# Performance work log

Measured on AMD Instinct MI355X. Metric: run time of the kernel, lower is better.

Reference implementation:

```python
import jax, jax.numpy as jnp
import numpy as np

B, T, X, H, Z, Y, G = 4096, 32, 256, 256, 128, 2, 128


def setup_inputs() -> dict:
    key = jax.random.key(0)
    ks = jax.random.split(key, 16)
    rn = lambda k, s, sc=0.05: jax.random.normal(k, s, dtype=jnp.float32) * sc
    n_days = jnp.concatenate([jnp.array([T], dtype=jnp.int32),
                              jax.random.randint(ks[2], (B - 1,), 1, T + 1).astype(jnp.int32)])
    return {
        "x": rn(ks[0], (B, T, X), 1.0),
        "y_true": jax.nn.softmax(jax.random.normal(ks[1], (B, T, Y), dtype=jnp.float32), axis=-1),
        "n_days": n_days,
        "z0": rn(ks[3], (B, Z), 1.0),
        "eps": rn(ks[4], (T, B, Z), 1.0),
        "W_ih": rn(ks[5], (3 * H, X)), "W_hh": rn(ks[6], (3 * H, H)),
        "b_ih": jnp.zeros((3 * H,), jnp.float32), "b_hh": jnp.zeros((3 * H,), jnp.float32),
        "Wph": rn(ks[7], (Z, X + H + Z)), "bph": jnp.zeros((Z,), jnp.float32),
        "Woh": rn(ks[8], (Z, X + H + Y + Z)), "boh": jnp.zeros((Z,), jnp.float32),
        "Wpm": rn(ks[9], (Z, Z)), "bpm": jnp.zeros((Z,), jnp.float32),
        "Wps": rn(ks[10], (Z, Z)), "bps": jnp.zeros((Z,), jnp.float32),
        "Wqm": rn(ks[11], (Z, Z)), "bqm": jnp.zeros((Z,), jnp.float32),
        "Wqs": rn(ks[12], (Z, Z)), "bqs": jnp.zeros((Z,), jnp.float32),
        "Wg": rn(ks[13], (G, H + Z)), "bg": jnp.zeros((G,), jnp.float32),
        "Wy": rn(ks[14], (Y, G)), "by": jnp.zeros((Y,), jnp.float32),
    }


def _forward(x, y_true, z0, eps, W_ih, W_hh, b_ih, b_hh, Wph, bph, Woh, boh,
             Wpm, bpm, Wps, bps, Wqm, bqm, Wqs, bqs, Wg, bg, Wy, by, n_days):
    xt = jnp.transpose(x, (1, 0, 2))       # [T, B, X]
    yt = jnp.transpose(y_true, (1, 0, 2))  # [T, B, Y]

    # --- GRU over time (torch nn.GRU gate math) ---
    def gru_step(h, xi):
        gi = xi @ W_ih.T + b_ih
        gh = h @ W_hh.T + b_hh
        ir, iz, inn = jnp.split(gi, 3, axis=-1)
        hr, hz, hn = jnp.split(gh, 3, axis=-1)
        r = jax.nn.sigmoid(ir + hr)
        u = jax.nn.sigmoid(iz + hz)
        n = jnp.tanh(inn + r * hn)
        h_new = (1.0 - u) * n + u * h
        return h_new, h_new

    h0 = jnp.zeros((x.shape[0], H), x.dtype)
    _, hs = jax.lax.scan(gru_step, h0, xt)  # [T, B, H]
    # pack/pad semantics: padded timesteps produce zero outputs
    valid = jnp.arange(T)[:, None] < n_days[None, :]  # [T, B]
    hs = jnp.where(valid[:, :, None], hs, 0.0)

    # --- sequential VAE latent scan: z_t depends on z_{t-1} ---
    def vmd_step(z, inputs):
        xi, hi, yi, ei = inputs
        hzp = jnp.tanh(jnp.concatenate([xi, hi, z], -1) @ Wph.T + bph)
        mp = hzp @ Wpm.T + bpm
        sp = jnp.sqrt(jnp.exp(hzp @ Wps.T + bps))
        hzq = jnp.tanh(jnp.concatenate([xi, hi, yi, z], -1) @ Woh.T + boh)
        mq = hzq @ Wqm.T + bqm
        sq = jnp.sqrt(jnp.exp(hzq @ Wqs.T + bqs))
        z_post = mq + sq * ei
        # kl_normal_normal(post || prior)
        kl = jnp.log(sp / sq) + (sq * sq + (mq - mp) ** 2) / (2.0 * sp * sp) - 0.5
        return z_post, (z_post, kl)

    _, (z_posts, kls_e) = jax.lax.scan(vmd_step, z0, (xt, hs, yt, eps))
    kls = jnp.sum(kls_e, axis=-1).T  # [B, T]

    hz = jnp.concatenate([jnp.transpose(hs, (1, 0, 2)),
                          jnp.transpose(z_posts, (1, 0, 2))], -1)  # [B, T, H+Z]
    g = jnp.tanh(hz @ Wg.T + bg)                     # [B, T, G]
    y_pred = jax.nn.softmax(g @ Wy.T + by, axis=-1)  # [B, T, Y]

    idx = n_days - 1
    b = jnp.arange(x.shape[0])
    g_T = g[b, idx]       # [B, G]
    y_T = y_pred[b, idx]  # [B, Y]
    return jnp.concatenate([g_T, y_T, kls], axis=-1)  # [B, G+Y+T]


def reference(x, y_true, n_days, z0, eps, W_ih, W_hh, b_ih, b_hh, Wph, bph,
              Woh, boh, Wpm, bpm, Wps, bps, Wqm, bqm, Wqs, bqs, Wg, bg, Wy, by):
    return _forward(x, y_true, z0, eps, W_ih, W_hh, b_ih, b_hh, Wph, bph, Woh,
                    boh, Wpm, bpm, Wps, bps, Wqm, bqm, Wqs, bqs, Wg, bg, Wy, by,
                    n_days)
```

## Files before the change

### kernel.cpp

```cpp
#include <hip/hip_runtime.h>

typedef unsigned short u16;
typedef short bf16x8 __attribute__((ext_vector_type(8)));
typedef float f32x4 __attribute__((ext_vector_type(4)));

__device__ __forceinline__ float bf2f(u16 v){
  union { unsigned u; float f; } x; x.u = ((unsigned)v) << 16; return x.f;
}
__device__ __forceinline__ u16 f2bf(float f){
  union { float f; unsigned u; } x; x.f = f;
  unsigned u = x.u;
  u += 0x7fffu + ((u >> 16) & 1u);
  return (u16)(u >> 16);
}
__device__ __forceinline__ unsigned pk_bf16(float lo, float hi){
  unsigned r;
  asm("v_cvt_pk_bf16_f32 %0, %1, %2" : "=v"(r) : "v"(lo), "v"(hi));
  return r;
}
__device__ __forceinline__ u16 el4(ushort4 v, int r){ return r==0?v.x:r==1?v.y:r==2?v.z:v.w; }
__device__ __forceinline__ float elf4(float4 v, int r){ return r==0?v.x:r==1?v.y:r==2?v.z:v.w; }
__device__ __forceinline__ float sigm(float x){ return 1.f/(1.f+__expf(-x)); }
__device__ __forceinline__ float tanh_s(float x){ return 1.f - 2.f/(__expf(2.f*x)+1.f); }
__device__ __forceinline__ f32x4 mfma16(bf16x8 a, bf16x8 b, f32x4 c){
  return __builtin_amdgcn_mfma_f32_16x16x32_bf16(a, b, c, 0, 0, 0);
}
__device__ __forceinline__ void gl2lds16(const void* g, void* l){
  __builtin_amdgcn_global_load_lds(
      (const __attribute__((address_space(1))) unsigned int*)g,
      (__attribute__((address_space(3))) unsigned int*)l, 16, 0, 0);
}

__global__ void prep_w(const float* __restrict__ W_ih, const float* __restrict__ W_hh,
                       const float* __restrict__ Wph, const float* __restrict__ Woh,
                       const float* __restrict__ Wpm, const float* __restrict__ Wps,
                       const float* __restrict__ Wqm, const float* __restrict__ Wqs,
                       const float* __restrict__ Wg,  const float* __restrict__ bph,
                       const float* __restrict__ boh,
                       u16* __restrict__ wsb, float* __restrict__ Woy, float* __restrict__ bpq)
{
  int idx = blockIdx.x*256 + threadIdx.x;
  if (idx < 196608){ wsb[idx] = f2bf(W_ih[idx]); return; }
  if (idx < 393216){ wsb[idx] = f2bf(W_hh[idx-196608]); return; }
  if (idx < 524288){ int j = idx-393216; int row = j>>9, col = j&511;
    float v = (row<128) ? Wph[row*640+col] : Woh[(row-128)*642+col];
    wsb[idx] = f2bf(v); return; }
  if (idx < 540672){ int j = idx-524288; int row=j>>7, col=j&127; wsb[idx]=f2bf(Wph[row*640+512+col]); return; }
  if (idx < 557056){ int j = idx-540672; int row=j>>7, col=j&127; wsb[idx]=f2bf(Woh[row*642+514+col]); return; }
  if (idx < 573440){ wsb[idx]=f2bf(Wpm[idx-557056]); return; }
  if (idx < 589824){ wsb[idx]=f2bf(Wps[idx-573440]); return; }
  if (idx < 606208){ wsb[idx]=f2bf(Wqm[idx-589824]); return; }
  if (idx < 622592){ wsb[idx]=f2bf(Wqs[idx-606208]); return; }
  if (idx < 671744){ wsb[idx]=f2bf(Wg[idx-622592]); return; }
  if (idx < 672000){ int j = idx-671744; int row=j>>1; Woy[j] = Woh[row*642+512+(j&1)]; return; }
  if (idx < 672256){ int j = idx-672000; bpq[j] = (j<128) ? bph[j] : boh[j-128]; return; }
}

__global__ void prep_b(const float* __restrict__ b_ih, const float* __restrict__ b_hh,
                       float* __restrict__ bsum)
{
  int j = threadIdx.x;
  if (j < 768) bsum[j] = b_ih[j] + (j < 512 ? b_hh[j] : 0.f);
}

__global__ void prep_x(const float* __restrict__ x, u16* __restrict__ xbf){
  int i = blockIdx.x*256 + threadIdx.x;
  if (i >= 4194304) return;
  const float4* src = (const float4*)(x + (size_t)i*8);
  float4 a = src[0], b = src[1];
  uint4 o;
  o.x = pk_bf16(a.x, a.y);
  o.y = pk_bf16(a.z, a.w);
  o.z = pk_bf16(b.x, b.y);
  o.w = pk_bf16(b.z, b.w);
  ((uint4*)xbf)[i] = o;
}

__global__ void sort_days(const int* __restrict__ n_days, int* __restrict__ perm,
                          int* __restrict__ nd_s, int* __restrict__ cnt)
{
  __shared__ int hist[34];
  __shared__ int base[34];
  __shared__ int cursor[34];
  int tid = threadIdx.x;
  if (tid < 34) hist[tid] = 0;
  __syncthreads();
  for (int i = tid; i < 4096; i += 1024) atomicAdd(&hist[n_days[i]], 1);
  __syncthreads();
  if (tid == 0){
    int acc = 0;
    for (int v = 32; v >= 1; --v){ base[v] = acc; acc += hist[v]; }
    base[0] = acc;
  }
  __syncthreads();
  if (tid < 33) cursor[tid] = base[tid];
  if (tid < 32) cnt[tid] = base[tid];
  __syncthreads();
  for (int i = tid; i < 4096; i += 1024){
    int v = n_days[i];
    int pos = atomicAdd(&cursor[v], 1);
    perm[pos] = i;
    nd_s[pos] = v;
  }
}

__global__ __launch_bounds__(512, 4) void gemm_gi(
  const u16* __restrict__ A, const u16* __restrict__ W,
  const float* __restrict__ bias, const int* __restrict__ perm,
  const int* __restrict__ cnt, u16* __restrict__ C)
{
  const int t  = blockIdx.x >> 5;
  const int rt = blockIdx.x & 31;
  if (rt*128 >= cnt[t]) return;
  const int n0 = blockIdx.y*256;
  const int tid = threadIdx.x;
  const int w = tid>>6, lane = tid&63, c = lane&15, g = lane>>4;
  const int wm = w>>2, wn = w&3;
  __shared__ __align__(16) char smem[49152];
  u16* abuf = (u16*)smem;
  u16* wbuf = (u16*)(smem + 16384);
  u16* clds = (u16*)smem;

  size_t asrc[2];
  #pragma unroll
  for (int i=0;i<2;++i){
    int p = (w*2+i)*64 + lane;
    int k8 = p>>7, row = p&127;
    asrc[i] = ((size_t)perm[rt*128 + row]*32 + t)*256 + k8*8;
  }
  size_t wsrc[4];
  #pragma unroll
  for (int i=0;i<4;++i){
    int p = (w*4+i)*64 + lane;
    int k8 = p>>8, row = p&255;
    wsrc[i] = (size_t)(n0+row)*256 + k8*8;
  }
  f32x4 acc[4][4];
  #pragma unroll
  for (int i=0;i<4;++i)
    #pragma unroll
    for (int j=0;j<4;++j) acc[i][j] = (f32x4){0.f,0.f,0.f,0.f};
  for (int kc=0; kc<4; ++kc){
    __syncthreads();
    #pragma unroll
    for (int i=0;i<2;++i) gl2lds16(A + asrc[i] + kc*64, &abuf[(w*2+i)*512]);
    #pragma unroll
    for (int i=0;i<4;++i) gl2lds16(W + wsrc[i] + kc*64, &wbuf[(w*4+i)*512]);
    __syncthreads();
    #pragma unroll
    for (int ks=0;ks<2;++ks){
      int k8 = ks*4 + g;
      bf16x8 a[4];
      #pragma unroll
      for (int mt=0;mt<4;++mt) a[mt] = *(const bf16x8*)&abuf[(k8*128 + wm*64 + mt*16 + c)*8];
      #pragma unroll
      for (int nt=0;nt<4;++nt){
        bf16x8 b = *(const bf16x8*)&wbuf[(k8*256 + wn*64 + nt*16 + c)*8];
        #pragma unroll
        for (int mt=0;mt<4;++mt)
          acc[mt][nt] = mfma16(a[mt], b, acc[mt][nt]);
      }
    }
  }
  __syncthreads();
  const size_t crow = (size_t)t*4096 + rt*128;
  #pragma unroll
  for (int nh=0; nh<2; ++nh){
    if ((wn>>1) == nh){
      #pragma unroll
      for (int nt=0;nt<4;++nt){
        int n = n0 + wn*64 + nt*16 + c;
        float bn = bias[n];
        int lc = (wn&1)*64 + nt*16 + c;
        #pragma unroll
        for (int mt=0;mt<4;++mt){
          int lr = wm*64 + mt*16 + g*4;
          #pragma unroll
          for (int r=0;r<4;++r)
            clds[(lr+r)*136 + lc] = f2bf(acc[mt][nt][r] + bn);
        }
      }
    }
    __syncthreads();
    #pragma unroll
    for (int p=0;p<4;++p){
      int idx = p*512 + tid;
      int row = idx>>4, ch = idx&15;
      *(uint4*)(C + (crow+row)*768 + n0 + nh*128 + ch*8)
        = *(const uint4*)&clds[row*136 + ch*8];
    }
    __syncthreads();
  }
}

__global__ __launch_bounds__(512, 4) void gemm_hpq(
  const u16* __restrict__ A1, const u16* __restrict__ A2,
  const u16* __restrict__ W, const float* __restrict__ bias,
  const float* __restrict__ yt, const float* __restrict__ Woy,
  u16* __restrict__ C)
{
  const int m0 = blockIdx.x*128;
  const int tid = threadIdx.x;
  const int w = tid>>6, lane = tid&63, c = lane&15, g = lane>>4;
  const int wm = w>>2, wn = w&3;
  __shared__ __align__(16) char smem[49152];
  u16* abuf = (u16*)smem;
  u16* wbuf = (u16*)(smem + 16384);
  u16* clds = (u16*)smem;

  size_t asrc[2];
  #pragma unroll
  for (int i=0;i<2;++i){
    int p = (w*2+i)*64 + lane;
    int k8 = p>>7, row = p&127;
    asrc[i] = (size_t)(m0+row)*256 + k8*8;
  }
  size_t wsrc[4];
  #pragma unroll
  for (int i=0;i<4;++i){
    int p = (w*4+i)*64 + lane;
    int k8 = p>>8, row = p&255;
    wsrc[i] = (size_t)row*512 + k8*8;
  }
  f32x4 acc[4][4];
  #pragma unroll
  for (int i=0;i<4;++i)
    #pragma unroll
    for (int j=0;j<4;++j) acc[i][j] = (f32x4){0.f,0.f,0.f,0.f};
  for (int kc=0; kc<8; ++kc){
    __syncthreads();
    const u16* Ab = (kc < 4) ? A1 : A2;
    int ko = (kc & 3)*64;
    #pragma unroll
    for (int i=0;i<2;++i) gl2lds16(Ab + asrc[i] + ko, &abuf[(w*2+i)*512]);
    #pragma unroll
    for (int i=0;i<4;++i) gl2lds16(W + wsrc[i] + kc*64, &wbuf[(w*4+i)*512]);
    __syncthreads();
    #pragma unroll
    for (int ks=0;ks<2;++ks){
      int k8 = ks*4 + g;
      bf16x8 a[4];
      #pragma unroll
      for (int mt=0;mt<4;++mt) a[mt] = *(const bf16x8*)&abuf[(k8*128 + wm*64 + mt*16 + c)*8];
      #pragma unroll
      for (int nt=0;nt<4;++nt){
        bf16x8 b = *(const bf16x8*)&wbuf[(k8*256 + wn*64 + nt*16 + c)*8];
        #pragma unroll
        for (int mt=0;mt<4;++mt)
          acc[mt][nt] = mfma16(a[mt], b, acc[mt][nt]);
      }
    }
  }
  __syncthreads();
  #pragma unroll
  for (int nh=0; nh<2; ++nh){
    if ((wn>>1) == nh){
      #pragma unroll
      for (int nt=0;nt<4;++nt){
        int n = wn*64 + nt*16 + c;
        float bn = bias[n];
        float wy0 = 0.f, wy1 = 0.f;
        bool yfl = (n >= 128);
        if (yfl){ wy0 = Woy[(n-128)*2]; wy1 = Woy[(n-128)*2+1]; }
        int lc = (wn&1)*64 + nt*16 + c;
        #pragma unroll
        for (int mt=0;mt<4;++mt){
          int lr = wm*64 + mt*16 + g*4;
          #pragma unroll
          for (int r=0;r<4;++r){
            size_t m = (size_t)m0 + lr + r;
            float v = acc[mt][nt][r] + bn;
            if (yfl) v += yt[2*m]*wy0 + yt[2*m+1]*wy1;
            clds[(lr+r)*136 + lc] = f2bf(v);
          }
        }
      }
    }
    __syncthreads();
    #pragma unroll
    for (int p=0;p<4;++p){
      int idx = p*512 + tid;
      int row = idx>>4, ch = idx&15;
      *(uint4*)(C + (size_t)(m0+row)*256 + nh*128 + ch*8)
        = *(const uint4*)&clds[row*136 + ch*8];
    }
    __syncthreads();
  }
}

__global__ __launch_bounds__(1024) void gru_seq(
  const u16* __restrict__ GI, const u16* __restrict__ Whh,
  const float* __restrict__ bhh, const int* __restrict__ perm,
  const int* __restrict__ nd_s, u16* __restrict__ hs)
{
  const int b0 = blockIdx.x*16;
  const int tid = threadIdx.x;
  const int w = tid>>6, lane = tid&63, c = lane&15, g = lane>>4;
  const int j0 = w*16 + g*4;
  __shared__ __align__(16) u16 hbuf[2][4096];

  bf16x8 wa[3][8];
  #pragma unroll
  for (int gate=0; gate<3; ++gate)
    #pragma unroll
    for (int ks=0; ks<8; ++ks)
      wa[gate][ks] = *(const bf16x8*)&Whh[(size_t)(gate*256 + w*16 + c)*256 + ks*32 + g*8];

  const float4 bhn4 = *(const float4*)(bhh + 512 + j0);
  const int ndc   = nd_s[b0 + c];
  const int bound = nd_s[b0];
  const int ob    = perm[b0 + c];

  const int hroff = (g*16 + c)*16;
  const int hwoff = ((w*2 + (g>>1))*16 + c)*16 + (g&1)*8;
  u16* hsp = hs + (size_t)ob*8192 + j0;
  const size_t PL = 3145728;
  const u16* gib = GI + (size_t)(b0+c)*768 + j0;

  float hprev[4] = {0.f,0.f,0.f,0.f};
  if (tid < 512) ((uint4*)hbuf[0])[tid] = make_uint4(0,0,0,0);

  ushort4 gA[3], gB[3];
  gA[0] = *(const ushort4*)(gib);
  gA[1] = *(const ushort4*)(gib + 256);
  gA[2] = *(const ushort4*)(gib + 512);
  {
    const u16* g1 = gib + ((bound > 1) ? PL : 0);
    gB[0] = *(const ushort4*)(g1);
    gB[1] = *(const ushort4*)(g1 + 256);
    gB[2] = *(const ushort4*)(g1 + 512);
  }
  __syncthreads();

  const u16* hr = hbuf[0];
  u16*       hw = hbuf[1];

  auto step = [&](ushort4 (&gs)[3], int t){
    f32x4 aR = (f32x4){0.f,0.f,0.f,0.f};
    f32x4 aU = (f32x4){0.f,0.f,0.f,0.f};
    f32x4 aN = (f32x4){bhn4.x, bhn4.y, bhn4.z, bhn4.w};
    __builtin_amdgcn_s_setprio(1);
    #pragma unroll
    for (int ks=0; ks<8; ++ks){
      bf16x8 hf = *(const bf16x8*)((const char*)hr + hroff + ks*1024);
      aR = mfma16(wa[0][ks], hf, aR);
      aU = mfma16(wa[1][ks], hf, aU);
      aN = mfma16(wa[2][ks], hf, aN);
    }
    __builtin_amdgcn_s_setprio(0);
    float h4[4];
    #pragma unroll
    for (int r=0; r<4; ++r){
      float rr = sigm(bf2f(el4(gs[0],r)) + aR[r]);
      float uu = sigm(bf2f(el4(gs[1],r)) + aU[r]);
      float nn = tanh_s(bf2f(el4(gs[2],r)) + rr*aN[r]);
      float h = nn + uu*(hprev[r]-nn);
      hprev[r] = h;
      h4[r] = h;
    }
    uint2 hpk;
    hpk.x = pk_bf16(h4[0], h4[1]);
    hpk.y = pk_bf16(h4[2], h4[3]);
    *(uint2*)((char*)hw + hwoff) = hpk;
    *(uint2*)(hsp + t*256) = (t < ndc) ? hpk : make_uint2(0u,0u);
    {
      int pf = (t+2 < bound) ? t+2 : bound-1;
      const u16* gp = gib + (size_t)pf*PL;
      gs[0] = *(const ushort4*)(gp);
      gs[1] = *(const ushort4*)(gp + 256);
      gs[2] = *(const ushort4*)(gp + 512);
    }
    asm volatile("s_waitcnt lgkmcnt(0)" ::: "memory");
    __builtin_amdgcn_sched_barrier(0);
    __builtin_amdgcn_s_barrier();
    __builtin_amdgcn_sched_barrier(0);
    const u16* tmp = hr; hr = hw; hw = (u16*)tmp;
  };

  int t = 0;
  for (;;){
    step(gA, t);
    if (++t >= bound) break;
    step(gB, t);
    if (++t >= bound) break;
  }
  for (int t2 = bound; t2 < 32; ++t2)
    *(uint2*)(hsp + t2*256) = make_uint2(0u,0u);
}

__global__ __launch_bounds__(512) void vae_seq(
  const u16* __restrict__ HPQ, const float* __restrict__ z0,
  const float* __restrict__ eps, const int* __restrict__ n_days,
  const u16* __restrict__ Wm,
  const float* __restrict__ bpm, const float* __restrict__ bps,
  const float* __restrict__ bqm, const float* __restrict__ bqs,
  u16* __restrict__ zidx, float* __restrict__ out)
{
  const int b0 = blockIdx.x*16;
  const int tid = threadIdx.x, w = tid>>6, lane = tid&63, c = lane&15, g = lane>>4;
  const int j0 = w*16 + g*4;
  __shared__ __align__(16) u16 zbuf[16*16*8];
  __shared__ __align__(16) u16 hzpb[16*16*8];
  __shared__ __align__(16) u16 hzqb[16*16*8];
  __shared__ float klb[32][16][8];

  bf16x8 wf[6][4];
  #pragma unroll
  for (int mat=0;mat<6;++mat)
    #pragma unroll
    for (int ks=0;ks<4;++ks)
      wf[mat][ks] = *(const bf16x8*)&Wm[mat*16384 + (w*16+c)*128 + ks*32 + g*8];

  const float4 bpm4 = *(const float4*)(bpm + j0);
  const float4 bps4 = *(const float4*)(bps + j0);
  const float4 bqm4 = *(const float4*)(bqm + j0);
  const float4 bqs4 = *(const float4*)(bqs + j0);
  const int ndc = n_days[b0 + c];

  const int hroff = (g*16 + c)*16;
  const int hwoff = ((w*2 + (g>>1))*16 + c)*16 + (g&1)*8;
  const u16*  hbp = HPQ + ((size_t)(b0+c)*32)*256 + j0;
  const float* ebp = eps + (size_t)(b0+c)*128 + j0;

  if (tid < 256){
    int k8 = tid>>4, row = tid&15;
    const float* zp = z0 + (size_t)(b0+row)*128 + k8*8;
    uint4 o;
    o.x = pk_bf16(zp[0], zp[1]);
    o.y = pk_bf16(zp[2], zp[3]);
    o.z = pk_bf16(zp[4], zp[5]);
    o.w = pk_bf16(zp[6], zp[7]);
    ((uint4*)zbuf)[tid] = o;
  }
  __syncthreads();

  ushort4 pA = *(const ushort4*)(hbp);
  ushort4 qA = *(const ushort4*)(hbp + 128);
  float4  eA = *(const float4*)(ebp);
  ushort4 pB = *(const ushort4*)(hbp + 256);
  ushort4 qB = *(const ushort4*)(hbp + 384);
  float4  eB = *(const float4*)(ebp + 524288);

  uint2 zsel = make_uint2(0u,0u);

  auto step = [&](ushort4& hp4, ushort4& hq4, float4& e4, int t){
    f32x4 accP = (f32x4){0,0,0,0}, accQ = (f32x4){0,0,0,0};
    #pragma unroll
    for (int ks=0;ks<4;++ks){
      bf16x8 zf = *(const bf16x8*)((const char*)zbuf + hroff + ks*1024);
      accP = mfma16(wf[0][ks], zf, accP);
      accQ = mfma16(wf[1][ks], zf, accQ);
    }
    float p4[4], q4[4];
    #pragma unroll
    for (int r=0;r<4;++r){
      p4[r] = tanh_s(bf2f(el4(hp4,r)) + accP[r]);
      q4[r] = tanh_s(bf2f(el4(hq4,r)) + accQ[r]);
    }
    uint2 ppk, qpk;
    ppk.x = pk_bf16(p4[0], p4[1]);  ppk.y = pk_bf16(p4[2], p4[3]);
    qpk.x = pk_bf16(q4[0], q4[1]);  qpk.y = pk_bf16(q4[2], q4[3]);
    *(uint2*)((char*)hzpb + hwoff) = ppk;
    *(uint2*)((char*)hzqb + hwoff) = qpk;
    asm volatile("s_waitcnt lgkmcnt(0)" ::: "memory");
    __builtin_amdgcn_sched_barrier(0);
    __builtin_amdgcn_s_barrier();
    __builtin_amdgcn_sched_barrier(0);
    f32x4 aMP=(f32x4){0,0,0,0}, aAP=(f32x4){0,0,0,0};
    f32x4 aMQ=(f32x4){0,0,0,0}, aAQ=(f32x4){0,0,0,0};
    #pragma unroll
    for (int ks=0;ks<4;++ks){
      bf16x8 pf = *(const bf16x8*)((const char*)hzpb + hroff + ks*1024);
      bf16x8 qf = *(const bf16x8*)((const char*)hzqb + hroff + ks*1024);
      aMP = mfma16(wf[2][ks], pf, aMP);
      aAP = mfma16(wf[3][ks], pf, aAP);
      aMQ = mfma16(wf[4][ks], qf, aMQ);
      aAQ = mfma16(wf[5][ks], qf, aAQ);
    }
    float kls = 0.f;
    float z4[4];
    #pragma unroll
    for (int r=0;r<4;++r){
      float mp = aMP[r]+elf4(bpm4,r);
      float ap = aAP[r]+elf4(bps4,r);
      float mq = aMQ[r]+elf4(bqm4,r);
      float aq = aAQ[r]+elf4(bqs4,r);
      float ev = elf4(e4,r);
      float z = mq + __expf(0.5f*aq)*ev;
      float d = mq - mp;
      kls += 0.5f*(ap-aq) + 0.5f*(__expf(aq)+d*d)*__expf(-ap) - 0.5f;
      z4[r] = z;
    }
    uint2 zpk;
    zpk.x = pk_bf16(z4[0], z4[1]);
    zpk.y = pk_bf16(z4[2], z4[3]);
    *(uint2*)((char*)zbuf + hwoff) = zpk;
    if (t == ndc-1) zsel = zpk;
    kls += __shfl_xor(kls, 16);
    kls += __shfl_xor(kls, 32);
    if (lane < 16) klb[t][c][w] = kls;
    if (t < 30){
      hp4 = *(const ushort4*)(hbp + (t+2)*256);
      hq4 = *(const ushort4*)(hbp + (t+2)*256 + 128);
      e4  = *(const float4*)(ebp + (size_t)(t+2)*524288);
    }
    asm volatile("s_waitcnt lgkmcnt(0)" ::: "memory");
    __builtin_amdgcn_sched_barrier(0);
    __builtin_amdgcn_s_barrier();
    __builtin_amdgcn_sched_barrier(0);
  };

  #pragma unroll 1
  for (int t=0; t<32; t+=2){
    step(pA, qA, eA, t);
    step(pB, qB, eB, t+1);
  }

  *(uint2*)(zidx + (size_t)(b0+c)*128 + j0) = zsel;
  {
    int t2 = tid>>4, c2 = tid&15;
    float s = 0.f;
    #pragma unroll
    for (int ww=0;ww<8;++ww) s += klb[t2][c2][ww];
    out[(size_t)(b0+c2)*162 + 130 + t2] = s;
  }
}

__global__ __launch_bounds__(128) void head_k(
  const u16* __restrict__ hs, const u16* __restrict__ zidx,
  const int* __restrict__ n_days, const u16* __restrict__ Wgb,
  const float* __restrict__ bg, const float* __restrict__ Wy,
  const float* __restrict__ by, float* __restrict__ out)
{
  const int b = blockIdx.x;
  const int tid = threadIdx.x;
  const int lane = tid & 63, wv = tid >> 6;
  __shared__ float hz[384];
  __shared__ float red[2][2];
  const int idx = n_days[b]-1;
  const u16* hrow = hs + ((size_t)b*32 + idx)*256;
  for (int k=tid; k<256; k+=128) hz[k] = bf2f(hrow[k]);
  hz[256+tid] = bf2f(zidx[(size_t)b*128 + tid]);
  __syncthreads();
  const u16* wrow = Wgb + (size_t)tid*384;
  float s = 0.f;
  #pragma unroll 4
  for (int k8=0;k8<48;++k8){
    bf16x8 wvv = *(const bf16x8*)&wrow[k8*8];
    #pragma unroll
    for (int e=0;e<8;++e) s += bf2f((u16)wvv[e]) * hz[k8*8+e];
  }
  float gv = tanh_s(s + bg[tid]);
  out[(size_t)b*162 + tid] = gv;
  float a0 = gv*Wy[tid], a1 = gv*Wy[128+tid];
  #pragma unroll
  for (int off=1; off<64; off<<=1){
    a0 += __shfl_xor(a0, off);
    a1 += __shfl_xor(a1, off);
  }
  if (lane == 0){ red[0][wv] = a0; red[1][wv] = a1; }
  __syncthreads();
  if (tid == 0){
    float l0 = by[0] + red[0][0] + red[0][1];
    float l1 = by[1] + red[1][0] + red[1][1];
    float mx = fmaxf(l0,l1);
    float e0 = __expf(l0-mx), e1 = __expf(l1-mx);
    float si = e0+e1;
    out[(size_t)b*162 + 128] = e0/si;
    out[(size_t)b*162 + 129] = e1/si;
  }
}

extern "C" void kernel_launch(void* const* d_in, const int* in_sizes, int n_in,
                              void* d_out, int out_size, void* d_ws, size_t ws_size,
                              hipStream_t stream)
{
  const float* x      = (const float*)d_in[0];
  const float* y_true = (const float*)d_in[1];
  const int*   n_days = (const int*)d_in[2];
  const float* z0     = (const float*)d_in[3];
  const float* eps    = (const float*)d_in[4];
  const float* W_ih   = (const float*)d_in[5];
  const float* W_hh   = (const float*)d_in[6];
  const float* b_ih   = (const float*)d_in[7];
  const float* b_hh   = (const float*)d_in[8];
  const float* Wph    = (const float*)d_in[9];
  const float* bph    = (const float*)d_in[10];
  const float* Woh    = (const float*)d_in[11];
  const float* boh    = (const float*)d_in[12];
  const float* Wpm    = (const float*)d_in[13];
  const float* bpm    = (const float*)d_in[14];
  const float* Wps    = (const float*)d_in[15];
  const float* bps    = (const float*)d_in[16];
  const float* Wqm    = (const float*)d_in[17];
  const float* bqm    = (const float*)d_in[18];
  const float* Wqs    = (const float*)d_in[19];
  const float* bqs    = (const float*)d_in[20];
  const float* Wg     = (const float*)d_in[21];
  const float* bg     = (const float*)d_in[22];
  const float* Wy     = (const float*)d_in[23];
  const float* by     = (const float*)d_in[24];
  (void)in_sizes; (void)n_in; (void)out_size; (void)ws_size;

  u16*   wsb = (u16*)d_ws;
  float* wsf = (float*)d_ws;
  int*   wsi = (int*)d_ws;
  u16* Wih_b = wsb + 0;
  u16* Whh_b = wsb + 196608;
  u16* Wc_b  = wsb + 393216;
  u16* Wz_b  = wsb + 524288;
  u16* Wg_b  = wsb + 622592;
  float* Woy  = wsf + 335872;
  float* bpq  = wsf + 336128;
  float* bsum = wsf + 336384;
  int* perm   = wsi + 337152;
  int* nd_s   = wsi + 341248;
  int* cnt    = wsi + 345344;
  u16* xbf   = wsb + 690752;
  u16* GI    = wsb + 34245184;
  u16* hsB   = wsb + 134908480;
  u16* HPQ   = wsb + 168462912;
  u16* zidx  = wsb + 202017344;

  hipLaunchKernelGGL(prep_w, dim3(2626), dim3(256), 0, stream,
                     W_ih, W_hh, Wph, Woh, Wpm, Wps, Wqm, Wqs, Wg, bph, boh,
                     wsb, Woy, bpq);
  hipLaunchKernelGGL(prep_b, dim3(1), dim3(768), 0, stream, b_ih, b_hh, bsum);
  hipLaunchKernelGGL(prep_x, dim3(16384), dim3(256), 0, stream, x, xbf);
  hipLaunchKernelGGL(sort_days, dim3(1), dim3(1024), 0, stream,
                     n_days, perm, nd_s, cnt);
  hipLaunchKernelGGL(gemm_gi, dim3(1024,3), dim3(512), 0, stream,
                     xbf, Wih_b, bsum, perm, cnt, GI);
  hipLaunchKernelGGL(gru_seq, dim3(256), dim3(1024), 0, stream,
                     GI, Whh_b, b_hh, perm, nd_s, hsB);
  hipLaunchKernelGGL(gemm_hpq, dim3(1024), dim3(512), 0, stream,
                     xbf, hsB, Wc_b, bpq, y_true, Woy, HPQ);
  hipLaunchKernelGGL(vae_seq, dim3(256), dim3(512), 0, stream,
                     HPQ, z0, eps, n_days, Wz_b, bpm, bps, bqm, bqs, zidx, (float*)d_out);
  hipLaunchKernelGGL(head_k, dim3(4096), dim3(128), 0, stream,
                     hsB, zidx, n_days, Wg_b, bg, Wy, by, (float*)d_out);
}
```

Baseline: 537.3 us.

## Coalesce GRU hidden-state stores via LDS readback and XOR-swizzle hbuf

The GRU kernel no longer writes each thread's scattered 4-element fragment of h to global memory. At the start of the next step each wave reads back one full batch row from the shared h buffer and writes it contiguously, so the stores are coalesced. The final step is flushed after the loop. The shared h buffer layout is XOR-swizzled on both the read and write sides to reduce LDS bank conflicts. This adds an extra LDS read per step and makes the indexing more complex. The vae_seq changes only rename variables and leave the behaviour the same.

```diff
diff --git a/kernel.cpp b/kernel.cpp
--- a/kernel.cpp
+++ b/kernel.cpp
@@ -307,13 +307,20 @@
       wa[gate][ks] = *(const bf16x8*)&Whh[(size_t)(gate*256 + w*16 + c)*256 + ks*32 + g*8];
 
   const float4 bhn4 = *(const float4*)(bhh + 512 + j0);
-  const int ndc   = nd_s[b0 + c];
   const int bound = nd_s[b0];
-  const int ob    = perm[b0 + c];
-
-  const int hroff = (g*16 + c)*16;
-  const int hwoff = ((w*2 + (g>>1))*16 + c)*16 + (g&1)*8;
-  u16* hsp = hs + (size_t)ob*8192 + j0;
+  const int ob_w  = perm[b0 + w];
+  const int ndc_w = nd_s[b0 + w];
+
+  const int hroffE = g*256 + ((c*16) ^ (g<<4));
+  const int hroffO = g*256 + ((c*16) ^ ((4+g)<<4));
+  {
+  }
+  const int hwk8  = w*2 + (g>>1);
+  const int hwoff = (hwk8*256 + c*16 + (g&1)*8) ^ ((hwk8&7)<<4);
+  const int rsk8  = lane>>1;
+  const int rsoff = (rsk8*256 + w*16 + (lane&1)*8) ^ ((rsk8&7)<<4);
+  u16* hrow_dst = hs + (size_t)ob_w*8192 + lane*4;
+
   const size_t PL = 3145728;
   const u16* gib = GI + (size_t)(b0+c)*768 + j0;
 
@@ -336,13 +343,18 @@
   u16*       hw = hbuf[1];
 
   auto step = [&](ushort4 (&gs)[3], int t){
+    if (t > 0){
+      uint2 hv = *(const uint2*)((const char*)hr + rsoff);
+      if (t-1 >= ndc_w) hv = make_uint2(0u,0u);
+      *(uint2*)(hrow_dst + (t-1)*256) = hv;
+    }
     f32x4 aR = (f32x4){0.f,0.f,0.f,0.f};
     f32x4 aU = (f32x4){0.f,0.f,0.f,0.f};
     f32x4 aN = (f32x4){bhn4.x, bhn4.y, bhn4.z, bhn4.w};
     __builtin_amdgcn_s_setprio(1);
     #pragma unroll
     for (int ks=0; ks<8; ++ks){
-      bf16x8 hf = *(const bf16x8*)((const char*)hr + hroff + ks*1024);
+      bf16x8 hf = *(const bf16x8*)((const char*)hr + ks*1024 + ((ks&1) ? hroffO : hroffE));
       aR = mfma16(wa[0][ks], hf, aR);
       aU = mfma16(wa[1][ks], hf, aU);
       aN = mfma16(wa[2][ks], hf, aN);
@@ -362,7 +374,6 @@
     hpk.x = pk_bf16(h4[0], h4[1]);
     hpk.y = pk_bf16(h4[2], h4[3]);
     *(uint2*)((char*)hw + hwoff) = hpk;
-    *(uint2*)(hsp + t*256) = (t < ndc) ? hpk : make_uint2(0u,0u);
     {
       int pf = (t+2 < bound) ? t+2 : bound-1;
       const u16* gp = gib + (size_t)pf*PL;
@@ -384,8 +395,13 @@
     step(gB, t);
     if (++t >= bound) break;
   }
+  {
+    uint2 hv = *(const uint2*)((const char*)hr + rsoff);
+    if (bound-1 >= ndc_w) hv = make_uint2(0u,0u);
+    *(uint2*)(hrow_dst + (bound-1)*256) = hv;
+  }
   for (int t2 = bound; t2 < 32; ++t2)
-    *(uint2*)(hsp + t2*256) = make_uint2(0u,0u);
+    *(uint2*)(hrow_dst + t2*256) = make_uint2(0u,0u);
 }
 
 __global__ __launch_bounds__(512) void vae_seq(
@@ -397,8 +413,9 @@
   u16* __restrict__ zidx, float* __restrict__ out)
 {
   const int b0 = blockIdx.x*16;
-  const int tid = threadIdx.x, w = tid>>6, lane = tid&63, c = lane&15, g = lane>>4;
-  const int j0 = w*16 + g*4;
+  const int tid = threadIdx.x, w = tid>>6, lane = tid&63, c = lane&15, g = tid>>4 & 3;
+  const int g2 = lane>>4;
+  const int j0 = w*16 + g2*4;
   __shared__ __align__(16) u16 zbuf[16*16*8];
   __shared__ __align__(16) u16 hzpb[16*16*8];
   __shared__ __align__(16) u16 hzqb[16*16*8];
@@ -409,7 +426,7 @@
   for (int mat=0;mat<6;++mat)
     #pragma unroll
     for (int ks=0;ks<4;++ks)
-      wf[mat][ks] = *(const bf16x8*)&Wm[mat*16384 + (w*16+c)*128 + ks*32 + g*8];
+      wf[mat][ks] = *(const bf16x8*)&Wm[mat*16384 + (w*16+c)*128 + ks*32 + g2*8];
 
   const float4 bpm4 = *(const float4*)(bpm + j0);
   const float4 bps4 = *(const float4*)(bps + j0);
@@ -417,8 +434,8 @@
   const float4 bqs4 = *(const float4*)(bqs + j0);
   const int ndc = n_days[b0 + c];
 
-  const int hroff = (g*16 + c)*16;
-  const int hwoff = ((w*2 + (g>>1))*16 + c)*16 + (g&1)*8;
+  const int hroff = (g2*16 + c)*16;
+  const int hwoff = ((w*2 + (g2>>1))*16 + c)*16 + (g2&1)*8;
   const u16*  hbp = HPQ + ((size_t)(b0+c)*32)*256 + j0;
   const float* ebp = eps + (size_t)(b0+c)*128 + j0;
 
```

After: 748.5 us. 1.39x slower.

## Double-buffer GEMM weight tiles and stage GRU gate inputs through LDS prefetch

Applied to the files above, without the earlier changes.

Both GEMM kernels now load the full A tile into LDS once and double-buffer the weight K-chunks, so the next chunk's global-to-LDS copy overlaps the MFMAs for the current one. gemm_hpq also halves its M tile to 64 rows and doubles its grid. The GRU recurrence moves its per-step gate-input loads from register prefetch into a 4-deep ring of swizzled LDS buffers, filled asynchronously three steps ahead with partial vmcnt waits. In exchange, the much larger LDS footprint (128 KB per GEMM block) lowers occupancy, and the new launch-bound hints could constrain register allocation in the GRU.

```diff
diff --git a/kernel.cpp b/kernel.cpp
--- a/kernel.cpp
+++ b/kernel.cpp
@@ -104,7 +104,7 @@
   }
 }
 
-__global__ __launch_bounds__(512, 4) void gemm_gi(
+__global__ __launch_bounds__(512, 2) void gemm_gi(
   const u16* __restrict__ A, const u16* __restrict__ W,
   const float* __restrict__ bias, const int* __restrict__ perm,
   const int* __restrict__ cnt, u16* __restrict__ C)
@@ -116,53 +116,62 @@
   const int tid = threadIdx.x;
   const int w = tid>>6, lane = tid&63, c = lane&15, g = lane>>4;
   const int wm = w>>2, wn = w&3;
-  __shared__ __align__(16) char smem[49152];
+  __shared__ __align__(16) char smem[131072];
   u16* abuf = (u16*)smem;
-  u16* wbuf = (u16*)(smem + 16384);
+  u16* wb0  = (u16*)(smem + 65536);
+  u16* wb1  = (u16*)(smem + 98304);
   u16* clds = (u16*)smem;
 
-  size_t asrc[2];
-  #pragma unroll
-  for (int i=0;i<2;++i){
-    int p = (w*2+i)*64 + lane;
-    int k8 = p>>7, row = p&127;
-    asrc[i] = ((size_t)perm[rt*128 + row]*32 + t)*256 + k8*8;
-  }
-  size_t wsrc[4];
+  #pragma unroll
+  for (int i=0;i<8;++i){
+    int p = w*8 + i;
+    int k8 = p>>1, row = (p&1)*64 + lane;
+    gl2lds16(A + ((size_t)perm[rt*128 + row]*32 + t)*256 + k8*8, abuf + p*512);
+  }
+  const u16* wsrc[4];
   #pragma unroll
   for (int i=0;i<4;++i){
-    int p = (w*4+i)*64 + lane;
-    int k8 = p>>8, row = p&255;
-    wsrc[i] = (size_t)(n0+row)*256 + k8*8;
-  }
+    int q = w*4 + i;
+    int k8 = q>>2, row = (q&3)*64 + lane;
+    wsrc[i] = W + (size_t)(n0+row)*256 + k8*8;
+  }
+  #pragma unroll
+  for (int i=0;i<4;++i) gl2lds16(wsrc[i], wb0 + (w*4+i)*512);
+  asm volatile("s_waitcnt vmcnt(0)" ::: "memory");
+  __syncthreads();
+
   f32x4 acc[4][4];
   #pragma unroll
   for (int i=0;i<4;++i)
     #pragma unroll
     for (int j=0;j<4;++j) acc[i][j] = (f32x4){0.f,0.f,0.f,0.f};
+
+  u16* wb[2] = {wb0, wb1};
+  int cur = 0;
+  #pragma unroll
   for (int kc=0; kc<4; ++kc){
-    __syncthreads();
-    #pragma unroll
-    for (int i=0;i<2;++i) gl2lds16(A + asrc[i] + kc*64, &abuf[(w*2+i)*512]);
-    #pragma unroll
-    for (int i=0;i<4;++i) gl2lds16(W + wsrc[i] + kc*64, &wbuf[(w*4+i)*512]);
-    __syncthreads();
+    int kn = (kc+1 < 4) ? kc+1 : kc;
+    #pragma unroll
+    for (int i=0;i<4;++i) gl2lds16(wsrc[i] + kn*64, wb[cur^1] + (w*4+i)*512);
     #pragma unroll
     for (int ks=0;ks<2;++ks){
-      int k8 = ks*4 + g;
+      int k8g = kc*8 + ks*4 + g;
       bf16x8 a[4];
       #pragma unroll
-      for (int mt=0;mt<4;++mt) a[mt] = *(const bf16x8*)&abuf[(k8*128 + wm*64 + mt*16 + c)*8];
+      for (int mt=0;mt<4;++mt) a[mt] = *(const bf16x8*)&abuf[(k8g*128 + wm*64 + mt*16 + c)*8];
       #pragma unroll
       for (int nt=0;nt<4;++nt){
-        bf16x8 b = *(const bf16x8*)&wbuf[(k8*256 + wn*64 + nt*16 + c)*8];
+        bf16x8 b = *(const bf16x8*)&wb[cur][((ks*4+g)*256 + wn*64 + nt*16 + c)*8];
         #pragma unroll
         for (int mt=0;mt<4;++mt)
           acc[mt][nt] = mfma16(a[mt], b, acc[mt][nt]);
       }
     }
-  }
-  __syncthreads();
+    asm volatile("s_waitcnt vmcnt(0)" ::: "memory");
+    __syncthreads();
+    cur ^= 1;
+  }
+
   const size_t crow = (size_t)t*4096 + rt*128;
   #pragma unroll
   for (int nh=0; nh<2; ++nh){
@@ -193,65 +202,73 @@
   }
 }
 
-__global__ __launch_bounds__(512, 4) void gemm_hpq(
+__global__ __launch_bounds__(512, 2) void gemm_hpq(
   const u16* __restrict__ A1, const u16* __restrict__ A2,
   const u16* __restrict__ W, const float* __restrict__ bias,
   const float* __restrict__ yt, const float* __restrict__ Woy,
   u16* __restrict__ C)
 {
-  const int m0 = blockIdx.x*128;
+  const int m0 = blockIdx.x*64;
   const int tid = threadIdx.x;
   const int w = tid>>6, lane = tid&63, c = lane&15, g = lane>>4;
   const int wm = w>>2, wn = w&3;
-  __shared__ __align__(16) char smem[49152];
+  __shared__ __align__(16) char smem[131072];
   u16* abuf = (u16*)smem;
-  u16* wbuf = (u16*)(smem + 16384);
+  u16* wb0  = (u16*)(smem + 65536);
+  u16* wb1  = (u16*)(smem + 98304);
   u16* clds = (u16*)smem;
 
-  size_t asrc[2];
-  #pragma unroll
-  for (int i=0;i<2;++i){
-    int p = (w*2+i)*64 + lane;
-    int k8 = p>>7, row = p&127;
-    asrc[i] = (size_t)(m0+row)*256 + k8*8;
-  }
-  size_t wsrc[4];
+  #pragma unroll
+  for (int i=0;i<8;++i){
+    int k8 = w*8 + i;
+    const u16* src = (k8 < 32) ? (A1 + (size_t)(m0+lane)*256 + k8*8)
+                               : (A2 + (size_t)(m0+lane)*256 + (k8-32)*8);
+    gl2lds16(src, abuf + (w*8+i)*512);
+  }
+  const u16* wsrc[4];
   #pragma unroll
   for (int i=0;i<4;++i){
-    int p = (w*4+i)*64 + lane;
-    int k8 = p>>8, row = p&255;
-    wsrc[i] = (size_t)row*512 + k8*8;
-  }
-  f32x4 acc[4][4];
-  #pragma unroll
-  for (int i=0;i<4;++i)
+    int q = w*4 + i;
+    int k8 = q>>2, row = (q&3)*64 + lane;
+    wsrc[i] = W + (size_t)row*512 + k8*8;
+  }
+  #pragma unroll
+  for (int i=0;i<4;++i) gl2lds16(wsrc[i], wb0 + (w*4+i)*512);
+  asm volatile("s_waitcnt vmcnt(0)" ::: "memory");
+  __syncthreads();
+
+  f32x4 acc[2][4];
+  #pragma unroll
+  for (int i=0;i<2;++i)
     #pragma unroll
     for (int j=0;j<4;++j) acc[i][j] = (f32x4){0.f,0.f,0.f,0.f};
+
+  u16* wb[2] = {wb0, wb1};
+  int cur = 0;
+  #pragma unroll
   for (int kc=0; kc<8; ++kc){
-    __syncthreads();
-    const u16* Ab = (kc < 4) ? A1 : A2;
-    int ko = (kc & 3)*64;
-    #pragma unroll
-    for (int i=0;i<2;++i) gl2lds16(Ab + asrc[i] + ko, &abuf[(w*2+i)*512]);
-    #pragma unroll
-    for (int i=0;i<4;++i) gl2lds16(W + wsrc[i] + kc*64, &wbuf[(w*4+i)*512]);
-    __syncthreads();
+    int kn = (kc+1 < 8) ? kc+1 : kc;
+    #pragma unroll
+    for (int i=0;i<4;++i) gl2lds16(wsrc[i] + kn*64, wb[cur^1] + (w*4+i)*512);
     #pragma unroll
     for (int ks=0;ks<2;++ks){
-      int k8 = ks*4 + g;
-      bf16x8 a[4];
+      int k8g = kc*8 + ks*4 + g;
+      bf16x8 a[2];
       #pragma unroll
-      for (int mt=0;mt<4;++mt) a[mt] = *(const bf16x8*)&abuf[(k8*128 + wm*64 + mt*16 + c)*8];
+      for (int mt=0;mt<2;++mt) a[mt] = *(const bf16x8*)&abuf[(k8g*64 + wm*32 + mt*16 + c)*8];
       #pragma unroll
       for (int nt=0;nt<4;++nt){
-        bf16x8 b = *(const bf16x8*)&wbuf[(k8*256 + wn*64 + nt*16 + c)*8];
+        bf16x8 b = *(const bf16x8*)&wb[cur][((ks*4+g)*256 + wn*64 + nt*16 + c)*8];
         #pragma unroll
-        for (int mt=0;mt<4;++mt)
+        for (int mt=0;mt<2;++mt)
           acc[mt][nt] = mfma16(a[mt], b, acc[mt][nt]);
       }
     }
-  }
-  __syncthreads();
+    asm volatile("s_waitcnt vmcnt(0)" ::: "memory");
+    __syncthreads();
+    cur ^= 1;
+  }
+
   #pragma unroll
   for (int nh=0; nh<2; ++nh){
     if ((wn>>1) == nh){
@@ -264,8 +281,8 @@
         if (yfl){ wy0 = Woy[(n-128)*2]; wy1 = Woy[(n-128)*2+1]; }
         int lc = (wn&1)*64 + nt*16 + c;
         #pragma unroll
-        for (int mt=0;mt<4;++mt){
-          int lr = wm*64 + mt*16 + g*4;
+        for (int mt=0;mt<2;++mt){
+          int lr = wm*32 + mt*16 + g*4;
           #pragma unroll
           for (int r=0;r<4;++r){
             size_t m = (size_t)m0 + lr + r;
@@ -278,7 +295,7 @@
     }
     __syncthreads();
     #pragma unroll
-    for (int p=0;p<4;++p){
+    for (int p=0;p<2;++p){
       int idx = p*512 + tid;
       int row = idx>>4, ch = idx&15;
       *(uint4*)(C + (size_t)(m0+row)*256 + nh*128 + ch*8)
@@ -288,7 +305,7 @@
   }
 }
 
-__global__ __launch_bounds__(1024) void gru_seq(
+__global__ __launch_bounds__(1024, 4) void gru_seq(
   const u16* __restrict__ GI, const u16* __restrict__ Whh,
   const float* __restrict__ bhh, const int* __restrict__ perm,
   const int* __restrict__ nd_s, u16* __restrict__ hs)
@@ -298,6 +315,7 @@
   const int w = tid>>6, lane = tid&63, c = lane&15, g = lane>>4;
   const int j0 = w*16 + g*4;
   __shared__ __align__(16) u16 hbuf[2][4096];
+  __shared__ __align__(16) u16 gibuf[4][12288];
 
   bf16x8 wa[3][8];
   #pragma unroll
@@ -311,31 +329,49 @@
   const int bound = nd_s[b0];
   const int ob    = perm[b0 + c];
 
+  int so0, so1;
+  { int pe = w*512 + lane*8; int row = pe/768, off = pe - row*768;
+    so0 = (b0+row)*768 + (off ^ ((row&7)<<3)); }
+  { int pe = (16+w)*512 + lane*8; int row = pe/768, off = pe - row*768;
+    so1 = (b0+row)*768 + (off ^ ((row&7)<<3)); }
+  const int rd0 = c*1536 + ((j0*2) ^ ((c&7)<<4));
   const int hroff = (g*16 + c)*16;
   const int hwoff = ((w*2 + (g>>1))*16 + c)*16 + (g&1)*8;
   u16* hsp = hs + (size_t)ob*8192 + j0;
-  const size_t PL = 3145728;
-  const u16* gib = GI + (size_t)(b0+c)*768 + j0;
 
   float hprev[4] = {0.f,0.f,0.f,0.f};
   if (tid < 512) ((uint4*)hbuf[0])[tid] = make_uint4(0,0,0,0);
 
-  ushort4 gA[3], gB[3];
-  gA[0] = *(const ushort4*)(gib);
-  gA[1] = *(const ushort4*)(gib + 256);
-  gA[2] = *(const ushort4*)(gib + 512);
-  {
-    const u16* g1 = gib + ((bound > 1) ? PL : 0);
-    gB[0] = *(const ushort4*)(g1);
-    gB[1] = *(const ushort4*)(g1 + 256);
-    gB[2] = *(const ushort4*)(g1 + 512);
-  }
+  const size_t PL = 3145728;
+  int p1 = (bound > 1) ? 1 : 0;
+  int p2 = (bound > 2) ? 2 : p1;
+  gl2lds16(GI + so0, (char*)gibuf[0] + w*1024);
+  if (w < 8) gl2lds16(GI + so1, (char*)gibuf[0] + (16+w)*1024);
+  gl2lds16(GI + (size_t)p1*PL + so0, (char*)gibuf[1] + w*1024);
+  if (w < 8) gl2lds16(GI + (size_t)p1*PL + so1, (char*)gibuf[1] + (16+w)*1024);
+  gl2lds16(GI + (size_t)p2*PL + so0, (char*)gibuf[2] + w*1024);
+  if (w < 8) gl2lds16(GI + (size_t)p2*PL + so1, (char*)gibuf[2] + (16+w)*1024);
+  asm volatile("s_waitcnt vmcnt(0)" ::: "memory");
   __syncthreads();
 
   const u16* hr = hbuf[0];
   u16*       hw = hbuf[1];
-
-  auto step = [&](ushort4 (&gs)[3], int t){
+  int cur = 0;
+  #pragma unroll 1
+  for (int t=0; t<bound; ++t){
+    {
+      int pf = (t+3 < bound) ? t+3 : bound-1;
+      int nxt = (cur+3)&3;
+      gl2lds16(GI + (size_t)pf*PL + so0, (char*)gibuf[nxt] + w*1024);
+      if (w < 8) gl2lds16(GI + (size_t)pf*PL + so1, (char*)gibuf[nxt] + (16+w)*1024);
+    }
+    const char* gib = (const char*)gibuf[cur];
+    ushort4 gr_ = *(const ushort4*)(gib + rd0);
+    ushort4 gu_ = *(const ushort4*)(gib + rd0 + 512);
+    ushort4 gn_ = *(const ushort4*)(gib + rd0 + 1024);
+    if (w < 8) asm volatile("s_waitcnt vmcnt(6)" ::: "memory");
+    else       asm volatile("s_waitcnt vmcnt(4)" ::: "memory");
+    __builtin_amdgcn_sched_barrier(0);
     f32x4 aR = (f32x4){0.f,0.f,0.f,0.f};
     f32x4 aU = (f32x4){0.f,0.f,0.f,0.f};
     f32x4 aN = (f32x4){bhn4.x, bhn4.y, bhn4.z, bhn4.w};
@@ -348,41 +384,30 @@
       aN = mfma16(wa[2][ks], hf, aN);
     }
     __builtin_amdgcn_s_setprio(0);
-    float h4[4];
-    #pragma unroll
-    for (int r=0; r<4; ++r){
-      float rr = sigm(bf2f(el4(gs[0],r)) + aR[r]);
-      float uu = sigm(bf2f(el4(gs[1],r)) + aU[r]);
-      float nn = tanh_s(bf2f(el4(gs[2],r)) + rr*aN[r]);
-      float h = nn + uu*(hprev[r]-nn);
-      hprev[r] = h;
-      h4[r] = h;
-    }
-    uint2 hpk;
-    hpk.x = pk_bf16(h4[0], h4[1]);
-    hpk.y = pk_bf16(h4[2], h4[3]);
-    *(uint2*)((char*)hw + hwoff) = hpk;
-    *(uint2*)(hsp + t*256) = (t < ndc) ? hpk : make_uint2(0u,0u);
     {
-      int pf = (t+2 < bound) ? t+2 : bound-1;
-      const u16* gp = gib + (size_t)pf*PL;
-      gs[0] = *(const ushort4*)(gp);
-      gs[1] = *(const ushort4*)(gp + 256);
-      gs[2] = *(const ushort4*)(gp + 512);
+      float h4[4];
+      #pragma unroll
+      for (int r=0; r<4; ++r){
+        float rr = sigm(bf2f(el4(gr_,r)) + aR[r]);
+        float uu = sigm(bf2f(el4(gu_,r)) + aU[r]);
+        float nn = tanh_s(bf2f(el4(gn_,r)) + rr*aN[r]);
+        float h = nn + uu*(hprev[r]-nn);
+        hprev[r] = h;
+        h4[r] = h;
+      }
+      uint2 hpk;
+      hpk.x = pk_bf16(h4[0], h4[1]);
+      hpk.y = pk_bf16(h4[2], h4[3]);
+      *(uint2*)((char*)hw + hwoff) = hpk;
+      uint2 hst = (t < ndc) ? hpk : make_uint2(0u,0u);
+      *(uint2*)(hsp + t*256) = hst;
     }
     asm volatile("s_waitcnt lgkmcnt(0)" ::: "memory");
     __builtin_amdgcn_sched_barrier(0);
     __builtin_amdgcn_s_barrier();
     __builtin_amdgcn_sched_barrier(0);
-    const u16* tmp = hr; hr = hw; hw = (u16*)tmp;
-  };
-
-  int t = 0;
-  for (;;){
-    step(gA, t);
-    if (++t >= bound) break;
-    step(gB, t);
-    if (++t >= bound) break;
+    { const u16* tmp = hr; hr = hw; hw = (u16*)tmp; }
+    cur = (cur+1)&3;
   }
   for (int t2 = bound; t2 < 32; ++t2)
     *(uint2*)(hsp + t2*256) = make_uint2(0u,0u);
@@ -397,8 +422,9 @@
   u16* __restrict__ zidx, float* __restrict__ out)
 {
   const int b0 = blockIdx.x*16;
-  const int tid = threadIdx.x, w = tid>>6, lane = tid&63, c = lane&15, g = lane>>4;
-  const int j0 = w*16 + g*4;
+  const int tid = threadIdx.x, w = tid>>6, lane = tid&63, c = lane&15;
+  const int g2 = lane>>4;
+  const int j0 = w*16 + g2*4;
   __shared__ __align__(16) u16 zbuf[16*16*8];
   __shared__ __align__(16) u16 hzpb[16*16*8];
   __shared__ __align__(16) u16 hzqb[16*16*8];
@@ -409,7 +435,7 @@
   for (int mat=0;mat<6;++mat)
     #pragma unroll
     for (int ks=0;ks<4;++ks)
-      wf[mat][ks] = *(const bf16x8*)&Wm[mat*16384 + (w*16+c)*128 + ks*32 + g*8];
+      wf[mat][ks] = *(const bf16x8*)&Wm[mat*16384 + (w*16+c)*128 + ks*32 + g2*8];
 
   const float4 bpm4 = *(const float4*)(bpm + j0);
   const float4 bps4 = *(const float4*)(bps + j0);
@@ -417,8 +443,8 @@
   const float4 bqs4 = *(const float4*)(bqs + j0);
   const int ndc = n_days[b0 + c];
 
-  const int hroff = (g*16 + c)*16;
-  const int hwoff = ((w*2 + (g>>1))*16 + c)*16 + (g&1)*8;
+  const int hroff = (g2*16 + c)*16;
+  const int hwoff = ((w*2 + (g2>>1))*16 + c)*16 + (g2&1)*8;
   const u16*  hbp = HPQ + ((size_t)(b0+c)*32)*256 + j0;
   const float* ebp = eps + (size_t)(b0+c)*128 + j0;
 
@@ -633,7 +659,7 @@
                      xbf, Wih_b, bsum, perm, cnt, GI);
   hipLaunchKernelGGL(gru_seq, dim3(256), dim3(1024), 0, stream,
                      GI, Whh_b, b_hh, perm, nd_s, hsB);
-  hipLaunchKernelGGL(gemm_hpq, dim3(1024), dim3(512), 0, stream,
+  hipLaunchKernelGGL(gemm_hpq, dim3(2048), dim3(512), 0, stream,
                      xbf, hsB, Wc_b, bpq, y_true, Woy, HPQ);
   hipLaunchKernelGGL(vae_seq, dim3(256), dim3(512), 0, stream,
                      HPQ, z0, eps, n_days, Wz_b, bpm, bps, bqm, bqs, zidx, (float*)d_out);
```

Result: slower. 574.5 us (+6.9%).

## Stage GRU input-gate slices through LDS with a 5-deep async prefetch ring

Applied to the files above, without the earlier changes.

The GRU recurrence kernel now loads each timestep's precomputed input-gate block for its 16 batch rows into a 5-slot shared-memory ring using direct global-to-LDS loads, prefetching four steps ahead with vmcnt-based waits. Before, each thread did small register-prefetched ushort4 global reads two steps ahead. The change aims to hide global memory latency on the serial critical path and to issue wider, coalesced loads, using an XOR swizzle to avoid bank conflicts. In exchange it adds about 120KB of LDS per block, a hand-tuned waitcnt scheme that is fragile, and launch bounds requesting extra occupancy. The vae_seq edit is only a variable rename.

```diff
diff --git a/kernel.cpp b/kernel.cpp
--- a/kernel.cpp
+++ b/kernel.cpp
@@ -288,7 +288,7 @@
   }
 }
 
-__global__ __launch_bounds__(1024) void gru_seq(
+__global__ __launch_bounds__(1024, 4) void gru_seq(
   const u16* __restrict__ GI, const u16* __restrict__ Whh,
   const float* __restrict__ bhh, const int* __restrict__ perm,
   const int* __restrict__ nd_s, u16* __restrict__ hs)
@@ -298,6 +298,7 @@
   const int w = tid>>6, lane = tid&63, c = lane&15, g = lane>>4;
   const int j0 = w*16 + g*4;
   __shared__ __align__(16) u16 hbuf[2][4096];
+  __shared__ __align__(16) u16 gibuf[5][12288];
 
   bf16x8 wa[3][8];
   #pragma unroll
@@ -311,31 +312,41 @@
   const int bound = nd_s[b0];
   const int ob    = perm[b0 + c];
 
+  int so0, so1;
+  { int pe = w*512 + lane*8; int row = pe/768, off = pe - row*768;
+    so0 = (b0+row)*768 + (off ^ ((row&7)<<3)); }
+  { int pe = (16+w)*512 + lane*8; int row = pe/768, off = pe - row*768;
+    so1 = (b0+row)*768 + (off ^ ((row&7)<<3)); }
+  const int rd0 = c*1536 + ((j0*2) ^ ((c&7)<<4));
   const int hroff = (g*16 + c)*16;
   const int hwoff = ((w*2 + (g>>1))*16 + c)*16 + (g&1)*8;
   u16* hsp = hs + (size_t)ob*8192 + j0;
-  const size_t PL = 3145728;
-  const u16* gib = GI + (size_t)(b0+c)*768 + j0;
 
   float hprev[4] = {0.f,0.f,0.f,0.f};
   if (tid < 512) ((uint4*)hbuf[0])[tid] = make_uint4(0,0,0,0);
 
-  ushort4 gA[3], gB[3];
-  gA[0] = *(const ushort4*)(gib);
-  gA[1] = *(const ushort4*)(gib + 256);
-  gA[2] = *(const ushort4*)(gib + 512);
-  {
-    const u16* g1 = gib + ((bound > 1) ? PL : 0);
-    gB[0] = *(const ushort4*)(g1);
-    gB[1] = *(const ushort4*)(g1 + 256);
-    gB[2] = *(const ushort4*)(g1 + 512);
-  }
+  const size_t PL = 3145728;
+  #pragma unroll
+  for (int p=0; p<4; ++p){
+    int pp = (p < bound) ? p : bound-1;
+    gl2lds16(GI + (size_t)pp*PL + so0, (char*)gibuf[p] + w*1024);
+    if (w < 8) gl2lds16(GI + (size_t)pp*PL + so1, (char*)gibuf[p] + (16+w)*1024);
+  }
+  asm volatile("s_waitcnt vmcnt(0)" ::: "memory");
   __syncthreads();
 
   const u16* hr = hbuf[0];
   u16*       hw = hbuf[1];
-
-  auto step = [&](ushort4 (&gs)[3], int t){
+  int cur = 0;
+  #pragma unroll 1
+  for (int t=0; t<bound; ++t){
+    if (w < 8) asm volatile("s_waitcnt vmcnt(9)" ::: "memory");
+    else       asm volatile("s_waitcnt vmcnt(6)" ::: "memory");
+    __builtin_amdgcn_sched_barrier(0);
+    const char* gib = (const char*)gibuf[cur];
+    ushort4 gr_ = *(const ushort4*)(gib + rd0);
+    ushort4 gu_ = *(const ushort4*)(gib + rd0 + 512);
+    ushort4 gn_ = *(const ushort4*)(gib + rd0 + 1024);
     f32x4 aR = (f32x4){0.f,0.f,0.f,0.f};
     f32x4 aU = (f32x4){0.f,0.f,0.f,0.f};
     f32x4 aN = (f32x4){bhn4.x, bhn4.y, bhn4.z, bhn4.w};
@@ -348,41 +359,38 @@
       aN = mfma16(wa[2][ks], hf, aN);
     }
     __builtin_amdgcn_s_setprio(0);
-    float h4[4];
-    #pragma unroll
-    for (int r=0; r<4; ++r){
-      float rr = sigm(bf2f(el4(gs[0],r)) + aR[r]);
-      float uu = sigm(bf2f(el4(gs[1],r)) + aU[r]);
-      float nn = tanh_s(bf2f(el4(gs[2],r)) + rr*aN[r]);
-      float h = nn + uu*(hprev[r]-nn);
-      hprev[r] = h;
-      h4[r] = h;
-    }
-    uint2 hpk;
-    hpk.x = pk_bf16(h4[0], h4[1]);
-    hpk.y = pk_bf16(h4[2], h4[3]);
-    *(uint2*)((char*)hw + hwoff) = hpk;
-    *(uint2*)(hsp + t*256) = (t < ndc) ? hpk : make_uint2(0u,0u);
     {
-      int pf = (t+2 < bound) ? t+2 : bound-1;
-      const u16* gp = gib + (size_t)pf*PL;
-      gs[0] = *(const ushort4*)(gp);
-      gs[1] = *(const ushort4*)(gp + 256);
-      gs[2] = *(const ushort4*)(gp + 512);
+      float h4[4];
+      #pragma unroll
+      for (int r=0; r<4; ++r){
+        float rr = sigm(bf2f(el4(gr_,r)) + aR[r]);
+        float uu = sigm(bf2f(el4(gu_,r)) + aU[r]);
+        float nn = tanh_s(bf2f(el4(gn_,r)) + rr*aN[r]);
+        float h = nn + uu*(hprev[r]-nn);
+        hprev[r] = h;
+        h4[r] = h;
+      }
+      uint2 hpk;
+      hpk.x = pk_bf16(h4[0], h4[1]);
+      hpk.y = pk_bf16(h4[2], h4[3]);
+      *(uint2*)((char*)hw + hwoff) = hpk;
+      uint2 hst = (t < ndc) ? hpk : make_uint2(0u,0u);
+      *(uint2*)(hsp + t*256) = hst;
+    }
+    __builtin_amdgcn_sched_barrier(0);
+    {
+      int pf = (t+4 < bound) ? t+4 : bound-1;
+      int nxt = cur;
+      nxt = cur >= 1 ? cur-1 : 4;
+      gl2lds16(GI + (size_t)pf*PL + so0, (char*)gibuf[nxt] + w*1024);
+      if (w < 8) gl2lds16(GI + (size_t)pf*PL + so1, (char*)gibuf[nxt] + (16+w)*1024);
     }
     asm volatile("s_waitcnt lgkmcnt(0)" ::: "memory");
     __builtin_amdgcn_sched_barrier(0);
     __builtin_amdgcn_s_barrier();
     __builtin_amdgcn_sched_barrier(0);
-    const u16* tmp = hr; hr = hw; hw = (u16*)tmp;
-  };
-
-  int t = 0;
-  for (;;){
-    step(gA, t);
-    if (++t >= bound) break;
-    step(gB, t);
-    if (++t >= bound) break;
+    { const u16* tmp = hr; hr = hw; hw = (u16*)tmp; }
+    cur = (cur == 4) ? 0 : cur+1;
   }
   for (int t2 = bound; t2 < 32; ++t2)
     *(uint2*)(hsp + t2*256) = make_uint2(0u,0u);
@@ -397,8 +405,9 @@
   u16* __restrict__ zidx, float* __restrict__ out)
 {
   const int b0 = blockIdx.x*16;
-  const int tid = threadIdx.x, w = tid>>6, lane = tid&63, c = lane&15, g = lane>>4;
-  const int j0 = w*16 + g*4;
+  const int tid = threadIdx.x, w = tid>>6, lane = tid&63, c = lane&15;
+  const int g2 = lane>>4;
+  const int j0 = w*16 + g2*4;
   __shared__ __align__(16) u16 zbuf[16*16*8];
   __shared__ __align__(16) u16 hzpb[16*16*8];
   __shared__ __align__(16) u16 hzqb[16*16*8];
@@ -409,7 +418,7 @@
   for (int mat=0;mat<6;++mat)
     #pragma unroll
     for (int ks=0;ks<4;++ks)
-      wf[mat][ks] = *(const bf16x8*)&Wm[mat*16384 + (w*16+c)*128 + ks*32 + g*8];
+      wf[mat][ks] = *(const bf16x8*)&Wm[mat*16384 + (w*16+c)*128 + ks*32 + g2*8];
 
   const float4 bpm4 = *(const float4*)(bpm + j0);
   const float4 bps4 = *(const float4*)(bps + j0);
@@ -417,8 +426,8 @@
   const float4 bqs4 = *(const float4*)(bqs + j0);
   const int ndc = n_days[b0 + c];
 
-  const int hroff = (g*16 + c)*16;
-  const int hwoff = ((w*2 + (g>>1))*16 + c)*16 + (g&1)*8;
+  const int hroff = (g2*16 + c)*16;
+  const int hwoff = ((w*2 + (g2>>1))*16 + c)*16 + (g2&1)*8;
   const u16*  hbp = HPQ + ((size_t)(b0+c)*32)*256 + j0;
   const float* ebp = eps + (size_t)(b0+c)*128 + j0;
 
```

New measurement: 489.8 us. 8.8% less time.
